# Optimization experiments

Hardware: AMD Instinct MI355X
Metric: run time of the kernel (lower is better)

Reference implementation:

```python
import jax, jax.numpy as jnp
import numpy as np

N_NODES = 100000


def gcn_conv(x, W, b, src, dst, n):
    # PyG GCNConv: linear transform, add self-loops, symmetric degree norm, scatter-add, bias
    h = x @ W                                      # [n, d_out]
    loop = jnp.arange(n, dtype=src.dtype)
    s = jnp.concatenate([src, loop])               # [E + n]
    d = jnp.concatenate([dst, loop])
    deg = jax.ops.segment_sum(jnp.ones_like(d, dtype=h.dtype), d, num_segments=n)
    dinv = jnp.where(deg > 0, jax.lax.rsqrt(deg), 0.0)
    norm = dinv[s] * dinv[d]                       # [E + n]
    msg = h[s] * norm[:, None]                     # gather + scale
    out = jax.ops.segment_sum(msg, d, num_segments=n)  # scatter-add over targets
    return out + b


def setup_inputs() -> dict:
    key = jax.random.key(0)
    ks = jax.random.split(key, 8)
    n, c_in, hid, c_out = N_NODES, 256, 128, 64
    x = jax.random.normal(ks[0], (n, c_in), dtype=jnp.float32)
    edge_index = jax.random.randint(ks[1], (2, 1600000), 0, n, dtype=jnp.int64)
    s = 0.1
    return {
        "x": x,
        "edge_index": edge_index,
        "W1": jax.random.normal(ks[2], (c_in, hid), dtype=jnp.float32) * s,
        "b1": jnp.zeros((hid,), dtype=jnp.float32),
        "Wmu": jax.random.normal(ks[3], (hid, c_out), dtype=jnp.float32) * s,
        "bmu": jnp.zeros((c_out,), dtype=jnp.float32),
        "Wlv": jax.random.normal(ks[4], (hid, c_out), dtype=jnp.float32) * s,
        "blv": jnp.zeros((c_out,), dtype=jnp.float32),
    }


def reference(x, edge_index, W1, b1, Wmu, bmu, Wlv, blv):
    n = x.shape[0]
    src, dst = edge_index[0], edge_index[1]
    h = jax.nn.relu(gcn_conv(x, W1, b1, src, dst, n))
    mu = gcn_conv(h, Wmu, bmu, src, dst, n)
    logvar = gcn_conv(h, Wlv, blv, src, dst, n)
    return mu, logvar
```

## Files before the change

kernel.cpp:

```cpp
#include <hip/hip_runtime.h>


#define C_IN  256
#define HID   128
#define C_OUT 64
#define NBUCK 1024
#define NSEG  256
#define CAPB  4096
#define EBCAP 4608

typedef __attribute__((ext_vector_type(8))) short bf16x8;
typedef __attribute__((ext_vector_type(4))) float f32x4;

__device__ inline unsigned short f2bf(float f) {
  unsigned u = __float_as_uint(f);
  unsigned r = u + 0x7FFF + ((u >> 16) & 1);
  return (unsigned short)(r >> 16);
}
__device__ inline float bflo(unsigned v) { return __uint_as_float(v << 16); }
__device__ inline float bfhi(unsigned v) { return __uint_as_float(v & 0xFFFF0000u); }

__global__ __launch_bounds__(1024) void k_seg_bin(
    const int* __restrict__ src, const int* __restrict__ dst, int E, int cap,
    int* __restrict__ cnt_arr, int* __restrict__ off_arr,
    unsigned* __restrict__ binned,
    const float* __restrict__ W1, const float* __restrict__ Wmu,
    const float* __restrict__ Wlv,
    unsigned short* __restrict__ bswz1, unsigned short* __restrict__ bswz2,
    unsigned* __restrict__ p1z, unsigned* __restrict__ p2z) {
  int tid = threadIdx.x;
  int wg = blockIdx.x;
  if (wg >= NSEG) {
    int idx = (wg - NSEG) * 1024 + tid;
    if (idx < 4096) {
      int L = idx & 63, t = (idx >> 6) & 7, s = idx >> 9;
      const float* srcp = W1 + (size_t)(s * 32 + ((L >> 4) << 3)) * 128 + t * 16 + (L & 15);
      unsigned short* dstp = bswz1 + (size_t)idx * 8;
#pragma unroll
      for (int j = 0; j < 8; j++) dstp[j] = f2bf(srcp[(size_t)j * 128]);
    } else if (idx < 6144) {
      int id2 = idx - 4096;
      int L = id2 & 63, t = (id2 >> 6) & 7, s = id2 >> 9;
      int nn = t * 16 + (L & 15);
      int k0 = s * 32 + ((L >> 4) << 3);
      const float* W = (nn < C_OUT) ? (Wmu + nn) : (Wlv + (nn - C_OUT));
      unsigned short* dstp = bswz2 + (size_t)id2 * 8;
#pragma unroll
      for (int j = 0; j < 8; j++) dstp[j] = f2bf(W[(size_t)(k0 + j) * C_OUT]);
    } else if (idx < 6208) {
      p1z[idx - 6144] = 0u;
    } else if (idx < 6272) {
      p2z[idx - 6208] = 0u;
    }
    return;
  }
  __shared__ int h[NBUCK], c[NBUCK];
  h[tid] = 0;
  __syncthreads();
  int e0 = wg * cap;
  int e1 = e0 + cap; if (e1 > E) e1 = E;
  for (int e = e0 + tid; e < e1; e += 1024)
    atomicAdd(&h[dst[e] >> 7], 1);
  __syncthreads();
  int v = h[tid];
  for (int ofs = 1; ofs < NBUCK; ofs <<= 1) {
    int add = (tid >= ofs) ? h[tid - ofs] : 0;
    __syncthreads();
    h[tid] += add;
    __syncthreads();
  }
  int excl = h[tid] - v;
  cnt_arr[(size_t)wg * NBUCK + tid] = v;
  off_arr[(size_t)wg * NBUCK + tid] = excl;
  c[tid] = excl;
  __syncthreads();
  for (int e = e0 + tid; e < e1; e += 1024) {
    int d = dst[e];
    int pos = e0 + atomicAdd(&c[d >> 7], 1);
    binned[pos] = (unsigned)src[e] | ((unsigned)(d & 127) << 17);
  }
}

__global__ __launch_bounds__(256) void k_bucket_build(
    const unsigned* __restrict__ binned, const int* __restrict__ cnt_arr,
    const int* __restrict__ off_arr, int cap,
    int* __restrict__ row_start, int* __restrict__ rdeg,
    float* __restrict__ dinv, int* __restrict__ csr, int n) {
  int b = blockIdx.x, t = threadIdx.x;
  __shared__ unsigned eb[EBCAP];
  __shared__ int sc[256];
  __shared__ int deg[128], ex[128], cur[128];
  int cnt = cnt_arr[(size_t)t * NBUCK + b];
  int off = off_arr[(size_t)t * NBUCK + b];
  sc[t] = cnt;
  __syncthreads();
  for (int ofs = 1; ofs < 256; ofs <<= 1) {
    int add = (t >= ofs) ? sc[t - ofs] : 0;
    __syncthreads();
    sc[t] += add;
    __syncthreads();
  }
  int lbase = sc[t] - cnt;
  int tot = sc[255];
  const unsigned* srcp = binned + (size_t)t * cap + off;
  for (int j = 0; j < cnt; ++j) {
    int ppos = lbase + j;
    if (ppos < EBCAP) eb[ppos] = srcp[j];
  }
  if (t < 128) deg[t] = 0;
  __syncthreads();
  if (tot > EBCAP) tot = EBCAP;
  for (int e = t; e < tot; e += 256)
    atomicAdd(&deg[eb[e] >> 17], 1);
  __syncthreads();
  if (t < 128) ex[t] = deg[t];
  __syncthreads();
  for (int ofs = 1; ofs < 128; ofs <<= 1) {
    int add = (t < 128 && t >= ofs) ? ex[t - ofs] : 0;
    __syncthreads();
    if (t < 128) ex[t] += add;
    __syncthreads();
  }
  if (t < 128) {
    int excl = ex[t] - deg[t];
    cur[t] = excl;
    int node = b * 128 + t;
    if (node < n) {
      row_start[node] = b * CAPB + excl;
      rdeg[node] = deg[t];
      dinv[node] = rsqrtf((float)deg[t] + 1.0f);
    }
  }
  __syncthreads();
  for (int e = t; e < tot; e += 256) {
    unsigned v = eb[e];
    int d = (int)(v >> 17);
    int pos = atomicAdd(&cur[d], 1);
    csr[(size_t)b * CAPB + pos] = (int)(v & 0x1FFFF);
  }
}

template <typename AT, int K>
__global__ __launch_bounds__(256) void k_gemm_mfma(const AT* __restrict__ A,
                                                   const unsigned short* __restrict__ bswz,
                                                   unsigned short* __restrict__ C,
                                                   const float* __restrict__ dinv,
                                                   int M) {
  constexpr int NS = K / 32;
  int wave = threadIdx.x >> 6, lane = threadIdx.x & 63;
  int m0 = blockIdx.x * 64 + wave * 16;
  int lrow = lane & 15, lq = lane >> 4;
  int arow = m0 + lrow;
  bool rv = arow < M;
  const AT* ap = A + (size_t)(rv ? arow : 0) * K + lq * 8;

  auto loadA = [&](int s) -> bf16x8 {
    if (sizeof(AT) == 4) {
      const float* af = (const float*)ap + s * 32;
      float4 u0 = rv ? *(const float4*)(af) : float4{0, 0, 0, 0};
      float4 u1 = rv ? *(const float4*)(af + 4) : float4{0, 0, 0, 0};
      union { unsigned short us[8]; bf16x8 v; } tmp;
      tmp.us[0] = f2bf(u0.x); tmp.us[1] = f2bf(u0.y);
      tmp.us[2] = f2bf(u0.z); tmp.us[3] = f2bf(u0.w);
      tmp.us[4] = f2bf(u1.x); tmp.us[5] = f2bf(u1.y);
      tmp.us[6] = f2bf(u1.z); tmp.us[7] = f2bf(u1.w);
      return tmp.v;
    } else {
      const unsigned short* ab = (const unsigned short*)ap + s * 32;
      return rv ? *(const bf16x8*)(ab) : (bf16x8)(short)0;
    }
  };

  f32x4 acc[8];
#pragma unroll
  for (int t = 0; t < 8; t++) acc[t] = (f32x4){0.f, 0.f, 0.f, 0.f};

  bf16x8 a_cur = loadA(0);
  bf16x8 b_cur[8];
#pragma unroll
  for (int t = 0; t < 8; t++)
    b_cur[t] = *(const bf16x8*)(bswz + lane * 8 + t * 512);

#pragma unroll
  for (int s = 0; s < NS; ++s) {
    bf16x8 a_nxt = a_cur;
    bf16x8 b_nxt[8];
    if (s + 1 < NS) {
      a_nxt = loadA(s + 1);
      const unsigned short* bp = bswz + (size_t)(s + 1) * 4096 + lane * 8;
#pragma unroll
      for (int t = 0; t < 8; t++) b_nxt[t] = *(const bf16x8*)(bp + t * 512);
    }
#pragma unroll
    for (int t = 0; t < 8; t++)
      acc[t] = __builtin_amdgcn_mfma_f32_16x16x32_bf16(a_cur, b_cur[t], acc[t], 0, 0, 0);
    a_cur = a_nxt;
    if (s + 1 < NS) {
#pragma unroll
      for (int t = 0; t < 8; t++) b_cur[t] = b_nxt[t];
    }
  }
#pragma unroll
  for (int i = 0; i < 4; i++) {
    int rr = m0 + lq * 4 + i;
    if (rr < M) {
      float dsc = dinv[rr];
      unsigned short* cp = C + (size_t)rr * 128 + lrow;
#pragma unroll
      for (int t = 0; t < 8; t++) cp[t * 16] = f2bf(acc[t][i] * dsc);
    }
  }
}

#define AGG_V4_BODY                                                                 \
  int tid = threadIdx.x;                                                            \
  int wid4 = blockIdx.x * 4 + (tid >> 6);                           \
  int lane = tid & 63;                                                              \
  int li = lane & 15;                                                               \
  int node = (wid4 << 2) + (lane >> 4);                                             \
  int rs = 0, re = -1;                                                              \
  if (node < n) { rs = row_start[node]; re = rs + rdeg[node]; }                     \
  int mc = re - rs + 1;                                       \
  mc = max(mc, __shfl_xor(mc, 16, 64));                                             \
  mc = max(mc, __shfl_xor(mc, 32, 64));                                             \
  int maxcnt = __builtin_amdgcn_readfirstlane(mc);                                  \
  const char* pb = (const char*)p;                                                  \
  unsigned loff = (unsigned)(li << 4);                                              \
  int vb = (lane & 48) << 2;          \
  float acc0 = 0.f, acc1 = 0.f, acc2 = 0.f, acc3 = 0.f;                             \
  float acc4 = 0.f, acc5 = 0.f, acc6 = 0.f, acc7 = 0.f;                             \
  for (int t0 = 0; t0 < maxcnt; t0 += 16) {                                         \
    int s = rs + t0 + li;                                                           \
    int sl = n;                                                       \
    if (s < re) sl = csr[s];                                                        \
    else if (s == re) sl = node;                                     \
    unsigned o[16];                                                                 \
    _Pragma("unroll")                                                               \
    for (int k = 0; k < 16; ++k)                                                    \
      o[k] = ((unsigned)__builtin_amdgcn_ds_bpermute(vb + (k << 2), sl)) << 8;      \
    uint4 v[16];                                                                    \
    _Pragma("unroll")                                                               \
    for (int k = 0; k < 16; ++k)                                                    \
      v[k] = *(const uint4*)(pb + (o[k] + loff));                                   \
    _Pragma("unroll")                                                               \
    for (int k = 0; k < 16; ++k) {                                                  \
      acc0 += bflo(v[k].x); acc1 += bfhi(v[k].x);                                   \
      acc2 += bflo(v[k].y); acc3 += bfhi(v[k].y);                                   \
      acc4 += bflo(v[k].z); acc5 += bfhi(v[k].z);                                   \
      acc6 += bflo(v[k].w); acc7 += bfhi(v[k].w);                                   \
    }                                                                               \
  }

__global__ __launch_bounds__(256) void k_agg_gemm2(
    const unsigned short* __restrict__ p, const float* __restrict__ dinv,
    const int* __restrict__ row_start, const int* __restrict__ rdeg,
    const int* __restrict__ csr,
    const float* __restrict__ bias, const unsigned short* __restrict__ bswz2,
    unsigned short* __restrict__ p2, int n) {
  __shared__ unsigned short hs[16][136];
  AGG_V4_BODY
  int rwg = ((tid >> 6) << 2) + (lane >> 4);
  {
    uint4 u = {0u, 0u, 0u, 0u};
    if (node < n) {
      float di = dinv[node];
      float4 ba = *(const float4*)(bias + (li << 3));
      float4 bb = *(const float4*)(bias + (li << 3) + 4);
      float r0 = fmaxf(acc0 * di + ba.x, 0.f);
      float r1 = fmaxf(acc1 * di + ba.y, 0.f);
      float r2 = fmaxf(acc2 * di + ba.z, 0.f);
      float r3 = fmaxf(acc3 * di + ba.w, 0.f);
      float r4 = fmaxf(acc4 * di + bb.x, 0.f);
      float r5 = fmaxf(acc5 * di + bb.y, 0.f);
      float r6 = fmaxf(acc6 * di + bb.z, 0.f);
      float r7 = fmaxf(acc7 * di + bb.w, 0.f);
      u.x = (unsigned)f2bf(r0) | ((unsigned)f2bf(r1) << 16);
      u.y = (unsigned)f2bf(r2) | ((unsigned)f2bf(r3) << 16);
      u.z = (unsigned)f2bf(r4) | ((unsigned)f2bf(r5) << 16);
      u.w = (unsigned)f2bf(r6) | ((unsigned)f2bf(r7) << 16);
    }
    *(uint4*)(&hs[rwg][li << 3]) = u;
  }
  __syncthreads();

  int w = tid >> 6;
  int lrow = lane & 15, lq = lane >> 4;
  f32x4 g0 = (f32x4){0.f, 0.f, 0.f, 0.f};
  f32x4 g1 = (f32x4){0.f, 0.f, 0.f, 0.f};
#pragma unroll
  for (int s = 0; s < 4; ++s) {
    bf16x8 af = *(const bf16x8*)(&hs[lrow][(lq << 3) + s * 32]);
    const unsigned short* bp = bswz2 + s * 4096 + (w * 2) * 512 + lane * 8;
    bf16x8 bf0 = *(const bf16x8*)(bp);
    bf16x8 bf1 = *(const bf16x8*)(bp + 512);
    g0 = __builtin_amdgcn_mfma_f32_16x16x32_bf16(af, bf0, g0, 0, 0, 0);
    g1 = __builtin_amdgcn_mfma_f32_16x16x32_bf16(af, bf1, g1, 0, 0, 0);
  }
#pragma unroll
  for (int i = 0; i < 4; ++i) {
    int rr = blockIdx.x * 16 + (lq << 2) + i;
    if (rr < n) {
      float dsc = dinv[rr];
      unsigned short* cp = p2 + (size_t)rr * 128 + lrow;
      cp[(w * 2) * 16]     = f2bf(g0[i] * dsc);
      cp[(w * 2 + 1) * 16] = f2bf(g1[i] * dsc);
    }
  }
}

__global__ __launch_bounds__(256) void k_agg_out_bf(
    const unsigned short* __restrict__ p, const float* __restrict__ dinv,
    const int* __restrict__ row_start, const int* __restrict__ rdeg,
    const int* __restrict__ csr,
    const float* __restrict__ bmu, const float* __restrict__ blv,
    float* __restrict__ out, int n) {
  AGG_V4_BODY
  if (node < n) {
    float di = dinv[node];
    const float* bp = (li < 8) ? (bmu + (li << 3)) : (blv + ((li - 8) << 3));
    float* op = (li < 8) ? (out + (size_t)node * C_OUT + (li << 3))
                         : (out + (size_t)(n + node) * C_OUT + ((li - 8) << 3));
    float4 b0 = *(const float4*)(bp);
    float4 b1 = *(const float4*)(bp + 4);
    float4 o0 = {acc0 * di + b0.x, acc1 * di + b0.y,
                 acc2 * di + b0.z, acc3 * di + b0.w};
    float4 o1 = {acc4 * di + b1.x, acc5 * di + b1.y,
                 acc6 * di + b1.z, acc7 * di + b1.w};
    *(float4*)op = o0;
    *(float4*)(op + 4) = o1;
  }
}

extern "C" void kernel_launch(void* const* d_in, const int* in_sizes, int n_in,
                              void* d_out, int out_size, void* d_ws, size_t ws_size,
                              hipStream_t stream) {
  const float* x   = (const float*)d_in[0];
  const int*   ei  = (const int*)d_in[1];
  const float* W1  = (const float*)d_in[2];
  const float* b1  = (const float*)d_in[3];
  const float* Wmu = (const float*)d_in[4];
  const float* bmu = (const float*)d_in[5];
  const float* Wlv = (const float*)d_in[6];
  const float* blv = (const float*)d_in[7];
  float* out = (float*)d_out;

  const int n = in_sizes[0] / C_IN;
  const int E = in_sizes[1] / 2;
  const int* src = ei;
  const int* dst = ei + E;

  char* w = (char*)d_ws;
  auto alloc = [&](size_t bytes) -> void* {
    void* pp = (void*)w;
    w += (bytes + 255) & ~(size_t)255;
    return pp;
  };
  float*          dinv       = (float*)alloc((size_t)n * 4);
  int*            row_start  = (int*)alloc((size_t)n * 4);
  int*            rdeg       = (int*)alloc((size_t)n * 4);
  int*            cnt_arr    = (int*)alloc((size_t)NSEG * NBUCK * 4);
  int*            off_arr    = (int*)alloc((size_t)NSEG * NBUCK * 4);
  unsigned*       binned     = (unsigned*)alloc((size_t)E * 4);
  int*            csr        = (int*)alloc((size_t)NBUCK * CAPB * 4);
  unsigned short* bswz1      = (unsigned short*)alloc((size_t)C_IN * 128 * 2);
  unsigned short* bswz2      = (unsigned short*)alloc((size_t)HID * 128 * 2);
  unsigned short* p1         = (unsigned short*)alloc((size_t)(n + 1) * 128 * 2);
  unsigned short* p2         = (unsigned short*)alloc((size_t)(n + 1) * 128 * 2);
  (void)ws_size; (void)n_in; (void)out_size;

  const int TB = 256;
  const int cap = (E + NSEG - 1) / NSEG;
  const int gemm_bks = (n + 63) / 64;
  const int agg_bks = (n + 15) / 16;
  const int nbk = (n + 127) / 128;

  k_seg_bin<<<NSEG + 7, 1024, 0, stream>>>(src, dst, E, cap, cnt_arr, off_arr,
                                           binned, W1, Wmu, Wlv, bswz1, bswz2,
                                           (unsigned*)(p1 + (size_t)n * 128),
                                           (unsigned*)(p2 + (size_t)n * 128));
  k_bucket_build<<<nbk, TB, 0, stream>>>(binned, cnt_arr, off_arr, cap,
                                         row_start, rdeg, dinv, csr, n);

  k_gemm_mfma<float, C_IN><<<gemm_bks, TB, 0, stream>>>(x, bswz1, p1, dinv, n);

  k_agg_gemm2<<<agg_bks, TB, 0, stream>>>(p1, dinv, row_start, rdeg, csr, b1,
                                          bswz2, p2, n);

  k_agg_out_bf<<<agg_bks, TB, 0, stream>>>(p2, dinv, row_start, rdeg, csr,
                                           bmu, blv, out, n);
}
```

Before: 362.5 us.

## Fuse CSR bucket build with first-layer GEMM by deferring source-side normalization

Merges the bucket-build kernel and the x@W1 GEMM into one launch with a block-index split. The GEMM no longer scales rows by dinv, so it can run alongside the degree computation. The source-side dinv factor is instead applied per edge in the first aggregation: each gathered neighbour's dinv is loaded and broadcast with ds_bpermute. This removes a kernel launch and a serialization point, at the cost of extra per-edge dinv loads and shuffles in the aggregation.

```diff
diff --git a/kernel.cpp b/kernel.cpp
--- a/kernel.cpp
+++ b/kernel.cpp
@@ -81,82 +81,81 @@
   }
 }
 
-__global__ __launch_bounds__(256) void k_bucket_build(
+__global__ __launch_bounds__(256) void k_build2(
     const unsigned* __restrict__ binned, const int* __restrict__ cnt_arr,
     const int* __restrict__ off_arr, int cap,
     int* __restrict__ row_start, int* __restrict__ rdeg,
-    float* __restrict__ dinv, int* __restrict__ csr, int n) {
-  int b = blockIdx.x, t = threadIdx.x;
+    float* __restrict__ dinv, int* __restrict__ csr, int n, int nbk,
+    const float* __restrict__ x, const unsigned short* __restrict__ bswz1,
+    unsigned short* __restrict__ p1) {
   __shared__ unsigned eb[EBCAP];
   __shared__ int sc[256];
   __shared__ int deg[128], ex[128], cur[128];
-  int cnt = cnt_arr[(size_t)t * NBUCK + b];
-  int off = off_arr[(size_t)t * NBUCK + b];
-  sc[t] = cnt;
-  __syncthreads();
-  for (int ofs = 1; ofs < 256; ofs <<= 1) {
-    int add = (t >= ofs) ? sc[t - ofs] : 0;
-    __syncthreads();
-    sc[t] += add;
-    __syncthreads();
-  }
-  int lbase = sc[t] - cnt;
-  int tot = sc[255];
-  const unsigned* srcp = binned + (size_t)t * cap + off;
-  for (int j = 0; j < cnt; ++j) {
-    int ppos = lbase + j;
-    if (ppos < EBCAP) eb[ppos] = srcp[j];
-  }
-  if (t < 128) deg[t] = 0;
-  __syncthreads();
-  if (tot > EBCAP) tot = EBCAP;
-  for (int e = t; e < tot; e += 256)
-    atomicAdd(&deg[eb[e] >> 17], 1);
-  __syncthreads();
-  if (t < 128) ex[t] = deg[t];
-  __syncthreads();
-  for (int ofs = 1; ofs < 128; ofs <<= 1) {
-    int add = (t < 128 && t >= ofs) ? ex[t - ofs] : 0;
-    __syncthreads();
-    if (t < 128) ex[t] += add;
-    __syncthreads();
-  }
-  if (t < 128) {
-    int excl = ex[t] - deg[t];
-    cur[t] = excl;
-    int node = b * 128 + t;
-    if (node < n) {
-      row_start[node] = b * CAPB + excl;
-      rdeg[node] = deg[t];
-      dinv[node] = rsqrtf((float)deg[t] + 1.0f);
-    }
-  }
-  __syncthreads();
-  for (int e = t; e < tot; e += 256) {
-    unsigned v = eb[e];
-    int d = (int)(v >> 17);
-    int pos = atomicAdd(&cur[d], 1);
-    csr[(size_t)b * CAPB + pos] = (int)(v & 0x1FFFF);
-  }
-}
-
-template <typename AT, int K>
-__global__ __launch_bounds__(256) void k_gemm_mfma(const AT* __restrict__ A,
-                                                   const unsigned short* __restrict__ bswz,
-                                                   unsigned short* __restrict__ C,
-                                                   const float* __restrict__ dinv,
-                                                   int M) {
-  constexpr int NS = K / 32;
-  int wave = threadIdx.x >> 6, lane = threadIdx.x & 63;
-  int m0 = blockIdx.x * 64 + wave * 16;
-  int lrow = lane & 15, lq = lane >> 4;
-  int arow = m0 + lrow;
-  bool rv = arow < M;
-  const AT* ap = A + (size_t)(rv ? arow : 0) * K + lq * 8;
-
-  auto loadA = [&](int s) -> bf16x8 {
-    if (sizeof(AT) == 4) {
-      const float* af = (const float*)ap + s * 32;
+  int t = threadIdx.x;
+  if ((int)blockIdx.x < nbk) {
+    int b = blockIdx.x;
+    int cnt = cnt_arr[(size_t)t * NBUCK + b];
+    int off = off_arr[(size_t)t * NBUCK + b];
+    sc[t] = cnt;
+    __syncthreads();
+    for (int ofs = 1; ofs < 256; ofs <<= 1) {
+      int add = (t >= ofs) ? sc[t - ofs] : 0;
+      __syncthreads();
+      sc[t] += add;
+      __syncthreads();
+    }
+    int lbase = sc[t] - cnt;
+    int tot = sc[255];
+    const unsigned* srcp = binned + (size_t)t * cap + off;
+    for (int j = 0; j < cnt; ++j) {
+      int ppos = lbase + j;
+      if (ppos < EBCAP) eb[ppos] = srcp[j];
+    }
+    if (t < 128) deg[t] = 0;
+    __syncthreads();
+    if (tot > EBCAP) tot = EBCAP;
+    for (int e = t; e < tot; e += 256)
+      atomicAdd(&deg[eb[e] >> 17], 1);
+    __syncthreads();
+    if (t < 128) ex[t] = deg[t];
+    __syncthreads();
+    for (int ofs = 1; ofs < 128; ofs <<= 1) {
+      int add = (t < 128 && t >= ofs) ? ex[t - ofs] : 0;
+      __syncthreads();
+      if (t < 128) ex[t] += add;
+      __syncthreads();
+    }
+    if (t < 128) {
+      int excl = ex[t] - deg[t];
+      cur[t] = excl;
+      int node = b * 128 + t;
+      if (node < n) {
+        row_start[node] = b * CAPB + excl;
+        rdeg[node] = deg[t];
+        dinv[node] = rsqrtf((float)deg[t] + 1.0f);
+      }
+    }
+    if (b == 0 && t == 0) dinv[n] = 0.f;
+    __syncthreads();
+    for (int e = t; e < tot; e += 256) {
+      unsigned v = eb[e];
+      int d = (int)(v >> 17);
+      int pos = atomicAdd(&cur[d], 1);
+      csr[(size_t)b * CAPB + pos] = (int)(v & 0x1FFFF);
+    }
+    return;
+  }
+  {
+    int chunk = (int)blockIdx.x - nbk;
+    int wave = t >> 6, lane = t & 63;
+    int lrow = lane & 15, lq = lane >> 4;
+    int m0 = chunk * 64 + wave * 16;
+    int arow = m0 + lrow;
+    bool rv = arow < n;
+    const float* ap = x + (size_t)(rv ? arow : 0) * C_IN + lq * 8;
+
+    auto loadA = [&](int s) -> bf16x8 {
+      const float* af = ap + s * 32;
       float4 u0 = rv ? *(const float4*)(af) : float4{0, 0, 0, 0};
       float4 u1 = rv ? *(const float4*)(af + 4) : float4{0, 0, 0, 0};
       union { unsigned short us[8]; bf16x8 v; } tmp;
@@ -165,52 +164,92 @@
       tmp.us[4] = f2bf(u1.x); tmp.us[5] = f2bf(u1.y);
       tmp.us[6] = f2bf(u1.z); tmp.us[7] = f2bf(u1.w);
       return tmp.v;
-    } else {
-      const unsigned short* ab = (const unsigned short*)ap + s * 32;
-      return rv ? *(const bf16x8*)(ab) : (bf16x8)(short)0;
-    }
-  };
-
-  f32x4 acc[8];
-#pragma unroll
-  for (int t = 0; t < 8; t++) acc[t] = (f32x4){0.f, 0.f, 0.f, 0.f};
-
-  bf16x8 a_cur = loadA(0);
-  bf16x8 b_cur[8];
-#pragma unroll
-  for (int t = 0; t < 8; t++)
-    b_cur[t] = *(const bf16x8*)(bswz + lane * 8 + t * 512);
-
-#pragma unroll
-  for (int s = 0; s < NS; ++s) {
-    bf16x8 a_nxt = a_cur;
-    bf16x8 b_nxt[8];
-    if (s + 1 < NS) {
-      a_nxt = loadA(s + 1);
-      const unsigned short* bp = bswz + (size_t)(s + 1) * 4096 + lane * 8;
-#pragma unroll
-      for (int t = 0; t < 8; t++) b_nxt[t] = *(const bf16x8*)(bp + t * 512);
-    }
-#pragma unroll
-    for (int t = 0; t < 8; t++)
-      acc[t] = __builtin_amdgcn_mfma_f32_16x16x32_bf16(a_cur, b_cur[t], acc[t], 0, 0, 0);
-    a_cur = a_nxt;
-    if (s + 1 < NS) {
-#pragma unroll
-      for (int t = 0; t < 8; t++) b_cur[t] = b_nxt[t];
-    }
-  }
-#pragma unroll
-  for (int i = 0; i < 4; i++) {
-    int rr = m0 + lq * 4 + i;
-    if (rr < M) {
-      float dsc = dinv[rr];
-      unsigned short* cp = C + (size_t)rr * 128 + lrow;
-#pragma unroll
-      for (int t = 0; t < 8; t++) cp[t * 16] = f2bf(acc[t][i] * dsc);
-    }
-  }
-}
+    };
+
+    f32x4 acc[8];
+#pragma unroll
+    for (int tt = 0; tt < 8; tt++) acc[tt] = (f32x4){0.f, 0.f, 0.f, 0.f};
+
+    bf16x8 a_cur = loadA(0);
+    bf16x8 b_cur[8];
+#pragma unroll
+    for (int tt = 0; tt < 8; tt++)
+      b_cur[tt] = *(const bf16x8*)(bswz1 + lane * 8 + tt * 512);
+
+#pragma unroll
+    for (int s = 0; s < C_IN / 32; ++s) {
+      bf16x8 a_nxt = a_cur;
+      bf16x8 b_nxt[8];
+      if (s + 1 < C_IN / 32) {
+        a_nxt = loadA(s + 1);
+        const unsigned short* bp = bswz1 + (size_t)(s + 1) * 4096 + lane * 8;
+#pragma unroll
+        for (int tt = 0; tt < 8; tt++) b_nxt[tt] = *(const bf16x8*)(bp + tt * 512);
+      }
+#pragma unroll
+      for (int tt = 0; tt < 8; tt++)
+        acc[tt] = __builtin_amdgcn_mfma_f32_16x16x32_bf16(a_cur, b_cur[tt], acc[tt], 0, 0, 0);
+      a_cur = a_nxt;
+      if (s + 1 < C_IN / 32) {
+#pragma unroll
+        for (int tt = 0; tt < 8; tt++) b_cur[tt] = b_nxt[tt];
+      }
+    }
+#pragma unroll
+    for (int i = 0; i < 4; i++) {
+      int rr = m0 + lq * 4 + i;
+      if (rr < n) {
+        unsigned short* cp = p1 + (size_t)rr * 128 + lrow;
+#pragma unroll
+        for (int tt = 0; tt < 8; tt++) cp[tt * 16] = f2bf(acc[tt][i]);
+      }
+    }
+  }
+}
+
+#define AGG_V4_W_BODY                                                               \
+  int tid = threadIdx.x;                                                            \
+  int wid4 = blockIdx.x * 4 + (tid >> 6);                           \
+  int lane = tid & 63;                                                              \
+  int li = lane & 15;                                                               \
+  int node = (wid4 << 2) + (lane >> 4);                                             \
+  int rs = 0, re = -1;                                                              \
+  if (node < n) { rs = row_start[node]; re = rs + rdeg[node]; }                     \
+  int mc = re - rs + 1;                                       \
+  mc = max(mc, __shfl_xor(mc, 16, 64));                                             \
+  mc = max(mc, __shfl_xor(mc, 32, 64));                                             \
+  int maxcnt = __builtin_amdgcn_readfirstlane(mc);                                  \
+  const char* pb = (const char*)p;                                                  \
+  unsigned loff = (unsigned)(li << 4);                                              \
+  int vb = (lane & 48) << 2;                                                        \
+  float acc0 = 0.f, acc1 = 0.f, acc2 = 0.f, acc3 = 0.f;                             \
+  float acc4 = 0.f, acc5 = 0.f, acc6 = 0.f, acc7 = 0.f;                             \
+  for (int t0 = 0; t0 < maxcnt; t0 += 16) {                                         \
+    int s = rs + t0 + li;                                                           \
+    int sl = n;                                             \
+    if (s < re) sl = csr[s];                                                        \
+    else if (s == re) sl = node;                                     \
+    int wb = __float_as_int(dinv[sl]);                                              \
+    unsigned o[16];                                                                 \
+    _Pragma("unroll")                                                               \
+    for (int k = 0; k < 16; ++k)                                                    \
+      o[k] = ((unsigned)__builtin_amdgcn_ds_bpermute(vb + (k << 2), sl)) << 8;      \
+    float wk[16];                                                                   \
+    _Pragma("unroll")                                                               \
+    for (int k = 0; k < 16; ++k)                                                    \
+      wk[k] = __int_as_float(__builtin_amdgcn_ds_bpermute(vb + (k << 2), wb));      \
+    uint4 v[16];                                                                    \
+    _Pragma("unroll")                                                               \
+    for (int k = 0; k < 16; ++k)                                                    \
+      v[k] = *(const uint4*)(pb + (o[k] + loff));                                   \
+    _Pragma("unroll")                                                               \
+    for (int k = 0; k < 16; ++k) {                                                  \
+      acc0 += bflo(v[k].x) * wk[k]; acc1 += bfhi(v[k].x) * wk[k];                   \
+      acc2 += bflo(v[k].y) * wk[k]; acc3 += bfhi(v[k].y) * wk[k];                   \
+      acc4 += bflo(v[k].z) * wk[k]; acc5 += bfhi(v[k].z) * wk[k];                   \
+      acc6 += bflo(v[k].w) * wk[k]; acc7 += bfhi(v[k].w) * wk[k];                   \
+    }                                                                               \
+  }
 
 #define AGG_V4_BODY                                                                 \
   int tid = threadIdx.x;                                                            \
@@ -226,7 +265,7 @@
   int maxcnt = __builtin_amdgcn_readfirstlane(mc);                                  \
   const char* pb = (const char*)p;                                                  \
   unsigned loff = (unsigned)(li << 4);                                              \
-  int vb = (lane & 48) << 2;          \
+  int vb = (lane & 48) << 2;                                                        \
   float acc0 = 0.f, acc1 = 0.f, acc2 = 0.f, acc3 = 0.f;                             \
   float acc4 = 0.f, acc5 = 0.f, acc6 = 0.f, acc7 = 0.f;                             \
   for (int t0 = 0; t0 < maxcnt; t0 += 16) {                                         \
@@ -258,7 +297,7 @@
     const float* __restrict__ bias, const unsigned short* __restrict__ bswz2,
     unsigned short* __restrict__ p2, int n) {
   __shared__ unsigned short hs[16][136];
-  AGG_V4_BODY
+  AGG_V4_W_BODY
   int rwg = ((tid >> 6) << 2) + (lane >> 4);
   {
     uint4 u = {0u, 0u, 0u, 0u};
@@ -355,7 +394,7 @@
     w += (bytes + 255) & ~(size_t)255;
     return pp;
   };
-  float*          dinv       = (float*)alloc((size_t)n * 4);
+  float*          dinv       = (float*)alloc((size_t)(n + 1) * 4);
   int*            row_start  = (int*)alloc((size_t)n * 4);
   int*            rdeg       = (int*)alloc((size_t)n * 4);
   int*            cnt_arr    = (int*)alloc((size_t)NSEG * NBUCK * 4);
@@ -378,10 +417,10 @@
                                            binned, W1, Wmu, Wlv, bswz1, bswz2,
                                            (unsigned*)(p1 + (size_t)n * 128),
                                            (unsigned*)(p2 + (size_t)n * 128));
-  k_bucket_build<<<nbk, TB, 0, stream>>>(binned, cnt_arr, off_arr, cap,
-                                         row_start, rdeg, dinv, csr, n);
-
-  k_gemm_mfma<float, C_IN><<<gemm_bks, TB, 0, stream>>>(x, bswz1, p1, dinv, n);
+
+  k_build2<<<nbk + gemm_bks, TB, 0, stream>>>(binned, cnt_arr, off_arr, cap,
+                                              row_start, rdeg, dinv, csr, n, nbk,
+                                              x, bswz1, p1);
 
   k_agg_gemm2<<<agg_bks, TB, 0, stream>>>(p1, dinv, row_start, rdeg, csr, b1,
                                           bswz2, p2, n);
```

Measured after the change: 363.5 us. Within noise of the previous version (+0.3%).
